# Kernel optimization log

Measured on AMD Instinct MI355X. Metric: run time of the kernel, lower is better.

The kernel has to match this reference:

```python
import jax, jax.numpy as jnp
import numpy as np

EMBED_DIM = 768
NUM_HEADS = 12
HEAD_DIM = EMBED_DIM // NUM_HEADS


def setup_inputs() -> dict:
    key = jax.random.key(0)
    ks = jax.random.split(key, 9)
    B, N, D = 1, 4096, EMBED_DIM
    s = 1.0 / np.sqrt(D)
    x = jax.random.normal(ks[0], (B, N, D), dtype=jnp.float32)
    Wq = jax.random.normal(ks[1], (D, D), dtype=jnp.float32) * s
    Wk = jax.random.normal(ks[2], (D, D), dtype=jnp.float32) * s
    Wv = jax.random.normal(ks[3], (D, D), dtype=jnp.float32) * s
    Wo = jax.random.normal(ks[4], (D, D), dtype=jnp.float32) * s
    bq = jax.random.normal(ks[5], (D,), dtype=jnp.float32) * 0.01
    bk = jax.random.normal(ks[6], (D,), dtype=jnp.float32) * 0.01
    bv = jax.random.normal(ks[7], (D,), dtype=jnp.float32) * 0.01
    bo = jax.random.normal(ks[8], (D,), dtype=jnp.float32) * 0.01
    return {"x": x, "Wq": Wq, "bq": bq, "Wk": Wk, "bk": bk,
            "Wv": Wv, "bv": bv, "Wo": Wo, "bo": bo}


def reference(x, Wq, bq, Wk, bk, Wv, bv, Wo, bo):
    B, N, D = x.shape
    h, d = NUM_HEADS, HEAD_DIM
    # projections; torch Linear computes x @ W.T + b, here W is stored as (in, out)
    q = (x @ Wq + bq).reshape(B, N, h, d).transpose(0, 2, 1, 3)  # [B,h,N,d]
    k = (x @ Wk + bk).reshape(B, N, h, d).transpose(0, 2, 1, 3)
    v = (x @ Wv + bv).reshape(B, N, h, d).transpose(0, 2, 1, 3)
    scores = jnp.einsum('bhnd,bhmd->bhnm', q, k) / np.sqrt(d)  # [B,h,N,N]
    attn = jax.nn.softmax(scores, axis=-1)
    out = jnp.einsum('bhnm,bhmd->bhnd', attn, v)  # [B,h,N,d]
    out = out.transpose(0, 2, 1, 3).reshape(B, N, D)
    return out @ Wo + bo
```

## Files before the change

kernel.cpp:

```cpp
#include <hip/hip_runtime.h>
#include <stdint.h>

#define EMBED 768
#define NTOK 4096
#define NHEAD 12
#define HD 64

typedef __attribute__((ext_vector_type(8))) short bf16x8;
typedef __attribute__((ext_vector_type(4))) float f32x4;
typedef __attribute__((ext_vector_type(16))) float f32x16;
typedef unsigned short ushort_t;

#define QSCALE 0.18033688011112042f

__device__ __forceinline__ unsigned short f2bf(float f) {
  union { float f; unsigned u; } c; c.f = f;
  unsigned u = c.u;
  u += 0x7fffu + ((u >> 16) & 1u);
  return (unsigned short)(u >> 16);
}

__device__ __forceinline__ void gld16(const void* g, void* l) {
  __builtin_amdgcn_global_load_lds((const __attribute__((address_space(1))) void*)g,
                                   (__attribute__((address_space(3))) void*)l,
                                   16, 0, 0);
}

__global__ void cvt_x_kernel(const float* __restrict__ x, ushort_t* __restrict__ xb) {
  size_t i = ((size_t)blockIdx.x * 256 + threadIdx.x) * 8;
  float4 a = *(const float4*)(x + i);
  float4 b = *(const float4*)(x + i + 4);
  uint4 p;
  p.x = (unsigned)f2bf(a.x) | ((unsigned)f2bf(a.y) << 16);
  p.y = (unsigned)f2bf(a.z) | ((unsigned)f2bf(a.w) << 16);
  p.z = (unsigned)f2bf(b.x) | ((unsigned)f2bf(b.y) << 16);
  p.w = (unsigned)f2bf(b.z) | ((unsigned)f2bf(b.w) << 16);
  *(uint4*)(xb + i) = p;
}

__global__ void transpose_w4_kernel(const float* __restrict__ w0, const float* __restrict__ w1,
                                    const float* __restrict__ w2, const float* __restrict__ w3,
                                    ushort_t* __restrict__ d0, ushort_t* __restrict__ d1,
                                    ushort_t* __restrict__ d2, ushort_t* __restrict__ d3) {
  __shared__ float t[32][33];
  int z = blockIdx.z;
  const float* w = (z == 0) ? w0 : (z == 1) ? w1 : (z == 2) ? w2 : w3;
  ushort_t* wt   = (z == 0) ? d0 : (z == 1) ? d1 : (z == 2) ? d2 : d3;
  int bx = blockIdx.x * 32, by = blockIdx.y * 32;
  int tx = threadIdx.x, ty = threadIdx.y;
  #pragma unroll
  for (int i = 0; i < 32; i += 8)
    t[ty + i][tx] = w[(size_t)(by + ty + i) * EMBED + bx + tx];
  __syncthreads();
  #pragma unroll
  for (int i = 0; i < 32; i += 8)
    wt[(size_t)(bx + ty + i) * EMBED + by + tx] = f2bf(t[tx][ty + i]);
}

template<int MODE>
__global__ __launch_bounds__(256)
void gemm_bt_kernel(const ushort_t* __restrict__ A, const ushort_t* __restrict__ Bt,
                    const float* __restrict__ b0, const float* __restrict__ b1,
                    const float* __restrict__ b2,
                    ushort_t* __restrict__ qo, ushort_t* __restrict__ ko,
                    ushort_t* __restrict__ vto, float* __restrict__ out) {
  __shared__ ushort_t As[128 * 32];
  __shared__ ushort_t Bs[128 * 32];
  const int K = EMBED;
  int tid = threadIdx.x, lane = tid & 63, wid = tid >> 6;
  int wy = wid >> 1, wx = wid & 1;
  int r0 = lane >> 4, cq = lane & 15;
  int brow = blockIdx.y * 128, bcol = blockIdx.x * 128;

  f32x4 acc[4][4] = {};

  for (int k0 = 0; k0 < K; k0 += 32) {
    #pragma unroll
    for (int c = 0; c < 2; ++c) {
      int chunk = wid * 2 + c;
      int eoff = chunk * 512;
      int le = eoff + lane * 8;
      int row = le >> 5, col = le & 31;
      gld16(A + (size_t)(brow + row) * K + k0 + col, As + eoff);
      gld16(Bt + (size_t)(bcol + row) * K + k0 + col, Bs + eoff);
    }
    __syncthreads();
    bf16x8 af[4], bfr[4];
    #pragma unroll
    for (int i = 0; i < 4; ++i)
      af[i] = *(const bf16x8*)(As + (wy * 64 + i * 16 + cq) * 32 + r0 * 8);
    #pragma unroll
    for (int i = 0; i < 4; ++i)
      bfr[i] = *(const bf16x8*)(Bs + (wx * 64 + i * 16 + cq) * 32 + r0 * 8);
    #pragma unroll
    for (int i = 0; i < 4; ++i)
      #pragma unroll
      for (int j = 0; j < 4; ++j)
        acc[i][j] = __builtin_amdgcn_mfma_f32_16x16x32_bf16(af[i], bfr[j], acc[i][j], 0, 0, 0);
    __syncthreads();
  }

  int sec = bcol / 768;
  int ncol0 = bcol - sec * 768;
  const float* bias = (sec == 0) ? b0 : (sec == 1) ? b1 : b2;
  #pragma unroll
  for (int i = 0; i < 4; ++i) {
    #pragma unroll
    for (int j = 0; j < 4; ++j) {
      #pragma unroll
      for (int jj = 0; jj < 4; ++jj) {
        int m = brow + wy * 64 + i * 16 + r0 * 4 + jj;
        int nn = ncol0 + wx * 64 + j * 16 + cq;
        float val = acc[i][j][jj] + bias[nn];
        if constexpr (MODE == 0) {
          int head = nn >> 6, dd = nn & 63;
          if (sec == 0)       qo[((size_t)head * NTOK + m) * HD + dd] = f2bf(val * QSCALE);
          else if (sec == 1)  ko[((size_t)head * NTOK + m) * HD + dd] = f2bf(val);
          else                vto[((size_t)head * HD + dd) * NTOK + m] = f2bf(val);
        } else {
          out[(size_t)m * EMBED + nn] = val;
        }
      }
    }
  }
}

__global__ __launch_bounds__(256, 2)
void flash_kernel(const ushort_t* __restrict__ q, const ushort_t* __restrict__ k,
                  const ushort_t* __restrict__ vt, ushort_t* __restrict__ o) {
  __shared__ float cmb[64 * 68 + 64];
  const int tid = threadIdx.x;
  const int lane = tid & 63;
  const int ks = tid >> 6;
  const int head = blockIdx.y;
  const int qbase = blockIdx.x * 64;
  const int c31 = lane & 31;
  const int hi = lane >> 5;

  const ushort_t* qh = q + (size_t)head * NTOK * HD;
  const ushort_t* kh = k + (size_t)head * NTOK * HD;
  const ushort_t* vh = vt + (size_t)head * HD * NTOK;

  bf16x8 qf[2][4];
  #pragma unroll
  for (int qt = 0; qt < 2; ++qt)
    #pragma unroll
    for (int dc = 0; dc < 4; ++dc)
      qf[qt][dc] = *(const bf16x8*)(qh + (size_t)(qbase + qt * 32 + c31) * HD + dc * 16 + hi * 8);

  f32x16 oacc[2][2] = {};
  float lsum[2] = {0.f, 0.f};

  bf16x8 kfr[8];
  {
    const ushort_t* kp = kh + (size_t)(ks * 64 + c31) * HD + hi * 8;
    #pragma unroll
    for (int kt = 0; kt < 2; ++kt)
      #pragma unroll
      for (int dc = 0; dc < 4; ++dc)
        kfr[kt * 4 + dc] = *(const bf16x8*)(kp + kt * 32 * HD + dc * 16);
  }

  for (int it = 0; it < 16; ++it) {
    const int kb = (ks + 4 * it) * 64;

    f32x16 s[2][2] = {};
    __builtin_amdgcn_s_setprio(1);
    #pragma unroll
    for (int dc = 0; dc < 4; ++dc)
      #pragma unroll
      for (int kt = 0; kt < 2; ++kt)
        #pragma unroll
        for (int qt = 0; qt < 2; ++qt)
          s[kt][qt] = __builtin_amdgcn_mfma_f32_32x32x16_bf16(kfr[kt * 4 + dc], qf[qt][dc], s[kt][qt], 0, 0, 0);
    __builtin_amdgcn_s_setprio(0);

    bf16x8 vfr[8];
    #pragma unroll
    for (int kc = 0; kc < 4; ++kc)
      #pragma unroll
      for (int dt = 0; dt < 2; ++dt)
        vfr[kc * 2 + dt] = *(const bf16x8*)(vh + (size_t)(dt * 32 + c31) * NTOK + kb + kc * 16 + hi * 8);

    if (it < 15) {
      const ushort_t* kp = kh + (size_t)((ks + 4 * (it + 1)) * 64 + c31) * HD + hi * 8;
      #pragma unroll
      for (int kt = 0; kt < 2; ++kt)
        #pragma unroll
        for (int dc = 0; dc < 4; ++dc)
          kfr[kt * 4 + dc] = *(const bf16x8*)(kp + kt * 32 * HD + dc * 16);
    }

    union pfu { unsigned u[4]; bf16x8 v; };
    pfu pf[2][4];
    #pragma unroll
    for (int qt = 0; qt < 2; ++qt) {
      unsigned w[2][8];
      #pragma unroll
      for (int kt = 0; kt < 2; ++kt) {
        float p[16];
        #pragma unroll
        for (int r = 0; r < 16; ++r)
          p[r] = __builtin_amdgcn_exp2f(s[kt][qt][r]);
        float s4[4];
        #pragma unroll
        for (int g = 0; g < 4; ++g)
          s4[g] = (p[4 * g] + p[4 * g + 1]) + (p[4 * g + 2] + p[4 * g + 3]);
        lsum[qt] += (s4[0] + s4[1]) + (s4[2] + s4[3]);
        #pragma unroll
        for (int m = 0; m < 8; ++m)
          asm("v_cvt_pk_bf16_f32 %0, %1, %2" : "=v"(w[kt][m]) : "v"(p[2 * m]), "v"(p[2 * m + 1]));
      }
      #pragma unroll
      for (int kc = 0; kc < 4; ++kc) {
        int kt = kc >> 1, kl = kc & 1;
        #pragma unroll
        for (int e = 0; e < 2; ++e) {
          unsigned a = w[kt][e + 4 * kl];
          unsigned b = w[kt][e + 4 * kl + 2];
          asm("v_permlane32_swap_b32 %0, %1" : "+v"(a), "+v"(b));
          pf[qt][kc].u[e] = a;
          pf[qt][kc].u[e + 2] = b;
        }
      }
    }

    __builtin_amdgcn_s_setprio(1);
    #pragma unroll
    for (int kc = 0; kc < 4; ++kc)
      #pragma unroll
      for (int dt = 0; dt < 2; ++dt)
        #pragma unroll
        for (int qt = 0; qt < 2; ++qt)
          oacc[dt][qt] = __builtin_amdgcn_mfma_f32_32x32x16_bf16(vfr[kc * 2 + dt], pf[qt][kc].v, oacc[dt][qt], 0, 0, 0);
    __builtin_amdgcn_s_setprio(0);
  }

  float* Oacc = cmb;
  float* lacc = cmb + 64 * 68;
  for (int t = tid; t < 64 * 68 + 64; t += 256)
    cmb[t] = 0.f;
  __syncthreads();
  #pragma unroll
  for (int qt = 0; qt < 2; ++qt) {
    int qq = qt * 32 + c31;
    atomicAdd(&lacc[qq], lsum[qt]);
    #pragma unroll
    for (int dt = 0; dt < 2; ++dt)
      #pragma unroll
      for (int g = 0; g < 4; ++g) {
        int dd = dt * 32 + 8 * g + 4 * hi;
        #pragma unroll
        for (int j = 0; j < 4; ++j)
          atomicAdd(&Oacc[qq * 68 + dd + j], oacc[dt][qt][4 * g + j]);
      }
  }
  __syncthreads();

  int qq = tid >> 2, seg = tid & 3;
  float linv = 1.0f / lacc[qq];
  unsigned outw[8];
  #pragma unroll
  for (int m = 0; m < 8; ++m) {
    float lo = Oacc[qq * 68 + seg * 16 + 2 * m] * linv;
    float hh = Oacc[qq * 68 + seg * 16 + 2 * m + 1] * linv;
    asm("v_cvt_pk_bf16_f32 %0, %1, %2" : "=v"(outw[m]) : "v"(lo), "v"(hh));
  }
  ushort_t* op = o + (size_t)(qbase + qq) * EMBED + head * HD + seg * 16;
  uint4 u0; u0.x = outw[0]; u0.y = outw[1]; u0.z = outw[2]; u0.w = outw[3];
  uint4 u1; u1.x = outw[4]; u1.y = outw[5]; u1.z = outw[6]; u1.w = outw[7];
  *(uint4*)op = u0;
  *((uint4*)op + 1) = u1;
}

extern "C" void kernel_launch(void* const* d_in, const int* in_sizes, int n_in,
                              void* d_out, int out_size, void* d_ws, size_t ws_size,
                              hipStream_t stream) {
  const float* x  = (const float*)d_in[0];
  const float* Wq = (const float*)d_in[1];
  const float* bq = (const float*)d_in[2];
  const float* Wk = (const float*)d_in[3];
  const float* bk = (const float*)d_in[4];
  const float* Wv = (const float*)d_in[5];
  const float* bv = (const float*)d_in[6];
  const float* Wo = (const float*)d_in[7];
  const float* bo = (const float*)d_in[8];
  float* out = (float*)d_out;

  char* ws = (char*)d_ws;
  ushort_t* xb    = (ushort_t*)ws;  ws += (size_t)NTOK * EMBED * 2;
  ushort_t* wqkvt = (ushort_t*)ws;  ws += (size_t)3 * EMBED * EMBED * 2;
  ushort_t* wot   = (ushort_t*)ws;  ws += (size_t)EMBED * EMBED * 2;
  ushort_t* qb    = (ushort_t*)ws;  ws += (size_t)NTOK * EMBED * 2;
  ushort_t* kb2   = (ushort_t*)ws;  ws += (size_t)NTOK * EMBED * 2;
  ushort_t* vtb   = (ushort_t*)ws;  ws += (size_t)NTOK * EMBED * 2;
  ushort_t* ao    = (ushort_t*)ws;  ws += (size_t)NTOK * EMBED * 2;

  cvt_x_kernel<<<(NTOK * EMBED) / (256 * 8), 256, 0, stream>>>(x, xb);
  transpose_w4_kernel<<<dim3(24, 24, 4), dim3(32, 8), 0, stream>>>(
      Wq, Wk, Wv, Wo,
      wqkvt, wqkvt + (size_t)EMBED * EMBED, wqkvt + (size_t)2 * EMBED * EMBED, wot);

  gemm_bt_kernel<0><<<dim3(2304 / 128, NTOK / 128), 256, 0, stream>>>(
      xb, wqkvt, bq, bk, bv, qb, kb2, vtb, nullptr);

  flash_kernel<<<dim3(NTOK / 64, NHEAD), 256, 0, stream>>>(qb, kb2, vtb, ao);

  gemm_bt_kernel<1><<<dim3(EMBED / 128, NTOK / 128), 256, 0, stream>>>(
      ao, wot, bo, nullptr, nullptr, nullptr, nullptr, nullptr, out);
}
```

Before: 288.5 us.

## Stage K/V tiles into swizzled LDS via async global_load_lds double buffering

Replaces per-wave direct global register loads of K and V fragments with asynchronous global-to-LDS copies into a per-wave double buffer, using XOR swizzles to avoid bank conflicts. The key tile per iteration is halved to 32 rows with twice as many iterations, and fragments are read from LDS right before each MFMA. This aims to hide global latency and cut register pressure from holding the kfr/vfr arrays. In exchange the kernel uses 64KB of LDS, which may limit occupancy to fewer blocks per CU, and adds more loop overhead.

```diff
diff --git a/kernel.cpp b/kernel.cpp
--- a/kernel.cpp
+++ b/kernel.cpp
@@ -125,10 +125,27 @@
   }
 }
 
+__device__ __forceinline__ void stage32(const ushort_t* kh, const ushort_t* vh,
+                                        int kb, char* buf, int lane) {
+  const int srow = lane >> 3, l7 = lane & 7;
+  const int ksl = l7 ^ srow;
+  const ushort_t* kg = kh + (size_t)kb * HD;
+  #pragma unroll
+  for (int i = 0; i < 4; ++i)
+    gld16(kg + ((i * 8 + srow) * HD + ksl * 8), buf + i * 1024);
+  char* vbuf = buf + 4096;
+  const int srw = lane >> 2;
+  const int vsl = (lane & 3) ^ (srw & 3);
+  const ushort_t* vg = vh + kb;
+  #pragma unroll
+  for (int i = 0; i < 4; ++i)
+    gld16(vg + ((size_t)(i * 16 + srw) * NTOK + vsl * 8), vbuf + i * 1024);
+}
+
 __global__ __launch_bounds__(256, 2)
 void flash_kernel(const ushort_t* __restrict__ q, const ushort_t* __restrict__ k,
                   const ushort_t* __restrict__ vt, ushort_t* __restrict__ o) {
-  __shared__ float cmb[64 * 68 + 64];
+  __shared__ __align__(16) char lds[65536];
   const int tid = threadIdx.x;
   const int lane = tid & 63;
   const int ks = tid >> 6;
@@ -141,6 +158,8 @@
   const ushort_t* kh = k + (size_t)head * NTOK * HD;
   const ushort_t* vh = vt + (size_t)head * HD * NTOK;
 
+  char* mybase = lds + ks * 16384;
+
   bf16x8 qf[2][4];
   #pragma unroll
   for (int qt = 0; qt < 2; ++qt)
@@ -151,73 +170,54 @@
   f32x16 oacc[2][2] = {};
   float lsum[2] = {0.f, 0.f};
 
-  bf16x8 kfr[8];
-  {
-    const ushort_t* kp = kh + (size_t)(ks * 64 + c31) * HD + hi * 8;
-    #pragma unroll
-    for (int kt = 0; kt < 2; ++kt)
-      #pragma unroll
-      for (int dc = 0; dc < 4; ++dc)
-        kfr[kt * 4 + dc] = *(const bf16x8*)(kp + kt * 32 * HD + dc * 16);
-  }
-
-  for (int it = 0; it < 16; ++it) {
-    const int kb = (ks + 4 * it) * 64;
-
-    f32x16 s[2][2] = {};
+  stage32(kh, vh, ks * 32, mybase, lane);
+
+  #pragma unroll 2
+  for (int it = 0; it < 32; ++it) {
+    const int cur = it & 1;
+    if (it < 31) {
+      stage32(kh, vh, (ks + 4 * (it + 1)) * 32, mybase + (cur ^ 1) * 8192, lane);
+      asm volatile("s_waitcnt vmcnt(8)" ::: "memory");
+    } else {
+      asm volatile("s_waitcnt vmcnt(0)" ::: "memory");
+    }
+    const char* kbuf = mybase + cur * 8192;
+    const char* vbuf = kbuf + 4096;
+
+    f32x16 s[2] = {};
     __builtin_amdgcn_s_setprio(1);
     #pragma unroll
-    for (int dc = 0; dc < 4; ++dc)
-      #pragma unroll
-      for (int kt = 0; kt < 2; ++kt)
-        #pragma unroll
-        for (int qt = 0; qt < 2; ++qt)
-          s[kt][qt] = __builtin_amdgcn_mfma_f32_32x32x16_bf16(kfr[kt * 4 + dc], qf[qt][dc], s[kt][qt], 0, 0, 0);
+    for (int dc = 0; dc < 4; ++dc) {
+      bf16x8 kf = *(const bf16x8*)(kbuf + c31 * 128 + (((dc * 2 + hi) ^ (c31 & 7)) * 16));
+      #pragma unroll
+      for (int qt = 0; qt < 2; ++qt)
+        s[qt] = __builtin_amdgcn_mfma_f32_32x32x16_bf16(kf, qf[qt][dc], s[qt], 0, 0, 0);
+    }
     __builtin_amdgcn_s_setprio(0);
 
-    bf16x8 vfr[8];
-    #pragma unroll
-    for (int kc = 0; kc < 4; ++kc)
-      #pragma unroll
-      for (int dt = 0; dt < 2; ++dt)
-        vfr[kc * 2 + dt] = *(const bf16x8*)(vh + (size_t)(dt * 32 + c31) * NTOK + kb + kc * 16 + hi * 8);
-
-    if (it < 15) {
-      const ushort_t* kp = kh + (size_t)((ks + 4 * (it + 1)) * 64 + c31) * HD + hi * 8;
-      #pragma unroll
-      for (int kt = 0; kt < 2; ++kt)
-        #pragma unroll
-        for (int dc = 0; dc < 4; ++dc)
-          kfr[kt * 4 + dc] = *(const bf16x8*)(kp + kt * 32 * HD + dc * 16);
-    }
-
     union pfu { unsigned u[4]; bf16x8 v; };
-    pfu pf[2][4];
+    pfu pf[2][2];
     #pragma unroll
     for (int qt = 0; qt < 2; ++qt) {
-      unsigned w[2][8];
-      #pragma unroll
-      for (int kt = 0; kt < 2; ++kt) {
-        float p[16];
-        #pragma unroll
-        for (int r = 0; r < 16; ++r)
-          p[r] = __builtin_amdgcn_exp2f(s[kt][qt][r]);
-        float s4[4];
-        #pragma unroll
-        for (int g = 0; g < 4; ++g)
-          s4[g] = (p[4 * g] + p[4 * g + 1]) + (p[4 * g + 2] + p[4 * g + 3]);
-        lsum[qt] += (s4[0] + s4[1]) + (s4[2] + s4[3]);
-        #pragma unroll
-        for (int m = 0; m < 8; ++m)
-          asm("v_cvt_pk_bf16_f32 %0, %1, %2" : "=v"(w[kt][m]) : "v"(p[2 * m]), "v"(p[2 * m + 1]));
-      }
-      #pragma unroll
-      for (int kc = 0; kc < 4; ++kc) {
-        int kt = kc >> 1, kl = kc & 1;
+      float p[16];
+      #pragma unroll
+      for (int r = 0; r < 16; ++r)
+        p[r] = __builtin_amdgcn_exp2f(s[qt][r]);
+      float s4[4];
+      #pragma unroll
+      for (int g = 0; g < 4; ++g)
+        s4[g] = (p[4 * g] + p[4 * g + 1]) + (p[4 * g + 2] + p[4 * g + 3]);
+      lsum[qt] += (s4[0] + s4[1]) + (s4[2] + s4[3]);
+      unsigned w[8];
+      #pragma unroll
+      for (int m = 0; m < 8; ++m)
+        asm("v_cvt_pk_bf16_f32 %0, %1, %2" : "=v"(w[m]) : "v"(p[2 * m]), "v"(p[2 * m + 1]));
+      #pragma unroll
+      for (int kc = 0; kc < 2; ++kc) {
         #pragma unroll
         for (int e = 0; e < 2; ++e) {
-          unsigned a = w[kt][e + 4 * kl];
-          unsigned b = w[kt][e + 4 * kl + 2];
+          unsigned a = w[e + 4 * kc];
+          unsigned b = w[e + 4 * kc + 2];
           asm("v_permlane32_swap_b32 %0, %1" : "+v"(a), "+v"(b));
           pf[qt][kc].u[e] = a;
           pf[qt][kc].u[e + 2] = b;
@@ -227,19 +227,22 @@
 
     __builtin_amdgcn_s_setprio(1);
     #pragma unroll
-    for (int kc = 0; kc < 4; ++kc)
-      #pragma unroll
-      for (int dt = 0; dt < 2; ++dt)
+    for (int kc = 0; kc < 2; ++kc)
+      #pragma unroll
+      for (int dt = 0; dt < 2; ++dt) {
+        bf16x8 vf = *(const bf16x8*)(vbuf + (dt * 32 + c31) * 64 + (((kc * 2 + hi) ^ (c31 & 3)) * 16));
         #pragma unroll
         for (int qt = 0; qt < 2; ++qt)
-          oacc[dt][qt] = __builtin_amdgcn_mfma_f32_32x32x16_bf16(vfr[kc * 2 + dt], pf[qt][kc].v, oacc[dt][qt], 0, 0, 0);
+          oacc[dt][qt] = __builtin_amdgcn_mfma_f32_32x32x16_bf16(vf, pf[qt][kc].v, oacc[dt][qt], 0, 0, 0);
+      }
     __builtin_amdgcn_s_setprio(0);
   }
 
-  float* Oacc = cmb;
-  float* lacc = cmb + 64 * 68;
+  __syncthreads();
+  float* Oacc = (float*)lds;
+  float* lacc = Oacc + 64 * 68;
   for (int t = tid; t < 64 * 68 + 64; t += 256)
-    cmb[t] = 0.f;
+    ((float*)lds)[t] = 0.f;
   __syncthreads();
   #pragma unroll
   for (int qt = 0; qt < 2; ++qt) {
```

Measured after the change: 265.0 us. 1.09x faster.
